# Kernel optimization log

Measured on AMD Instinct MI355X. Metric: run time of the kernel, lower is better.

## Reference

```python
import jax, jax.numpy as jnp
import numpy as np
from jax import lax

B, C_IN, C_OUT, T = 2048, 64, 64, 32
E = 32768
K_HOPS = 2
KSIZE = 3
EPS = 1e-5
SLOPE = 0.01  # torch LeakyReLU default negative_slope


def setup_inputs() -> dict:
    key = jax.random.key(0)
    ks = jax.random.split(key, 10)
    x = jax.random.normal(ks[0], (B, C_IN, T), dtype=jnp.float32)
    edge_index = jax.random.randint(ks[1], (2, E), 0, B, dtype=jnp.int64)
    edge_weight = jax.random.uniform(ks[2], (E,), dtype=jnp.float32)
    # temporal Conv1d params: weight [out, in, k], bias [out]
    conv_w = jax.random.normal(ks[3], (C_OUT, C_IN, KSIZE), dtype=jnp.float32) / np.sqrt(C_IN * KSIZE)
    conv_b = jnp.zeros((C_OUT,), dtype=jnp.float32)
    # LayerNorm([out_channels, T]) elementwise affine over last two dims
    ln_g = jnp.ones((C_OUT, T), dtype=jnp.float32)
    ln_b = jnp.zeros((C_OUT, T), dtype=jnp.float32)
    # BatchNorm1d over node features inside residual layer (res+ pre-norm)
    bn_g = jnp.ones((C_OUT,), dtype=jnp.float32)
    bn_b = jnp.zeros((C_OUT,), dtype=jnp.float32)
    # TAGConv: one linear per hop (K+1 of them) plus bias
    tag_w = jax.random.normal(ks[4], (K_HOPS + 1, C_OUT, C_OUT), dtype=jnp.float32) / np.sqrt(C_OUT)
    tag_b = jnp.zeros((C_OUT,), dtype=jnp.float32)
    return {
        'x': x, 'edge_index': edge_index, 'edge_weight': edge_weight,
        'conv_w': conv_w, 'conv_b': conv_b, 'ln_g': ln_g, 'ln_b': ln_b,
        'bn_g': bn_g, 'bn_b': bn_b, 'tag_w': tag_w, 'tag_b': tag_b,
    }


def _forward(x, edge_index, edge_weight, conv_w, conv_b, ln_g, ln_b, bn_g, bn_b, tag_w, tag_b):
    Bn, Cin, Tn = x.shape
    # --- Temporal1DConvLayer: Conv1d with padding=k-1 both sides, truncate to T, pool='none', LeakyReLU ---
    y = lax.conv_general_dilated(x, conv_w, window_strides=(1,),
                                 padding=[(KSIZE - 1, KSIZE - 1)],
                                 dimension_numbers=('NCH', 'OIH', 'NCH'))
    y = y + conv_b[None, :, None]
    y = y[..., :Tn]                                   # [B, C_out, T]
    y = jnp.where(y >= 0, y, SLOPE * y)               # LeakyReLU
    # --- temporal_norm_layer: LayerNorm over (C_out, T) jointly ---
    mu = jnp.mean(y, axis=(1, 2), keepdims=True)
    var = jnp.var(y, axis=(1, 2), keepdims=True)
    y = (y - mu) * lax.rsqrt(var + EPS) * ln_g[None] + ln_b[None]
    # --- parallelize over time: permute(2,0,1) -> [T, B, F]; edges replicated per t ---
    h_in = jnp.transpose(y, (2, 0, 1))                # [T, B, F]
    # --- ResidualLayer (res+): h = h_in + TAGConv(LeakyReLU(BatchNorm(h_in))) ---
    mu_n = jnp.mean(h_in, axis=(0, 1))                # batch stats over all T*B node copies
    var_n = jnp.var(h_in, axis=(0, 1))
    z = (h_in - mu_n) * lax.rsqrt(var_n + EPS) * bn_g + bn_b
    z = jnp.where(z >= 0, z, SLOPE * z)
    src, dst = edge_index[0], edge_index[1]
    out = jnp.einsum('tbf,fg->tbg', z, tag_w[0])
    p = z
    for k in range(1, K_HOPS + 1):
        msg = p[:, src, :] * edge_weight[None, :, None]   # [T, E, F] gather
        p = jnp.zeros_like(p).at[:, dst, :].add(msg)      # scatter-add per timestep
        out = out + jnp.einsum('tbf,fg->tbg', p, tag_w[k])
    out = out + tag_b
    h = h_in + out                                    # residual 'res+'
    # --- reshape back: [T, B, F] -> [B, F, T] ---
    return jnp.transpose(h, (1, 2, 0))


def reference(x, edge_index, edge_weight, conv_w, conv_b, ln_g, ln_b, bn_g, bn_b, tag_w, tag_b):
    return _forward(x, edge_index, edge_weight, conv_w, conv_b, ln_g, ln_b, bn_g, bn_b, tag_w, tag_b)
```

## Files before the change

### kernel.cpp

```cpp
#include <hip/hip_runtime.h>
#include <cstddef>

#define NB   2048
#define NE   32768
#define NTC  2048
#define SLOPE_F 0.01f
#define EPS_F   1e-5f

typedef short bf16x8 __attribute__((ext_vector_type(8)));
typedef float f32x4  __attribute__((ext_vector_type(4)));

__device__ __forceinline__ unsigned short f2bf(float f) {
    unsigned u = __builtin_bit_cast(unsigned, f);
    u += 0x7FFF + ((u >> 16) & 1);
    return (unsigned short)(u >> 16);
}
__device__ __forceinline__ float bflo(unsigned v) {
    return __builtin_bit_cast(float, v << 16);
}
__device__ __forceinline__ float bfhi(unsigned v) {
    return __builtin_bit_cast(float, v & 0xFFFF0000u);
}
__device__ __forceinline__ unsigned pk2(float lo, float hi) {
    return (unsigned)f2bf(lo) | ((unsigned)f2bf(hi) << 16);
}
__device__ __forceinline__ void accv8(float* acc, const uint4& v, float wt) {
    acc[0] += wt * bflo(v.x); acc[1] += wt * bfhi(v.x);
    acc[2] += wt * bflo(v.y); acc[3] += wt * bfhi(v.y);
    acc[4] += wt * bflo(v.z); acc[5] += wt * bfhi(v.z);
    acc[6] += wt * bflo(v.w); acc[7] += wt * bfhi(v.w);
}
__device__ __forceinline__ void acci16(float* acc, const uint4& v, float wt) {
    acc[0] += wt * (float)(short)(v.x & 0xFFFFu); acc[1] += wt * (float)(short)(v.x >> 16);
    acc[2] += wt * (float)(short)(v.y & 0xFFFFu); acc[3] += wt * (float)(short)(v.y >> 16);
    acc[4] += wt * (float)(short)(v.z & 0xFFFFu); acc[5] += wt * (float)(short)(v.z >> 16);
    acc[6] += wt * (float)(short)(v.w & 0xFFFFu); acc[7] += wt * (float)(short)(v.w >> 16);
}
__device__ __forceinline__ unsigned pkq2(float a, float b, float inv) {
    int qa = __float2int_rn(a * inv);
    int qb = __float2int_rn(b * inv);
    return ((unsigned)qa & 0xFFFFu) | ((unsigned)qb << 16);
}
__device__ __forceinline__ void spl2(float a, float b, unsigned& hw, unsigned& lw) {
    unsigned short ha = f2bf(a), hb = f2bf(b);
    float ra = a - bflo((unsigned)ha);
    float rb = b - bflo((unsigned)hb);
    hw = (unsigned)ha | ((unsigned)hb << 16);
    lw = (unsigned)f2bf(ra) | ((unsigned)f2bf(rb) << 16);
}

__device__ __forceinline__ int edge_src(const int* ei, int m, int e) {
    return m ? ei[e] : ei[2 * e];
}
__device__ __forceinline__ int edge_dst(const int* ei, int m, int e) {
    return m ? ei[NE + e] : ei[2 * (NE + e)];
}

__global__ __launch_bounds__(256)
void k_pre(int* __restrict__ hist, const float* __restrict__ cw,
           unsigned short* __restrict__ wAb, const float* __restrict__ tw,
           unsigned short* __restrict__ twB, unsigned short* __restrict__ twBlo)
{
    int gid = blockIdx.x * 256 + threadIdx.x;
    if (gid < 2048) hist[gid] = 0;
    if (blockIdx.x < 48) {
        int idx = gid;
        int kk = idx >> 12, o = (idx >> 6) & 63, i = idx & 63;
        wAb[idx] = f2bf(cw[o * 192 + i * 3 + kk]);
    } else if (blockIdx.x < 96) {
        int idx = gid - 48 * 256;
        int mm = idx >> 12, rem = idx & 4095;
        int g = rem >> 6, k = rem & 63;
        twB[idx] = f2bf(tw[mm * 4096 + k * 64 + g]);
    } else {
        int idx = gid - 96 * 256;
        int g = idx >> 6, k = idx & 63;
        float v = tw[2 * 4096 + k * 64 + g];
        unsigned short hi = f2bf(v);
        twBlo[idx] = f2bf(v - bflo((unsigned)hi));
    }
}

__global__ __launch_bounds__(256, 4)
void k_main(const float* __restrict__ x, const unsigned short* __restrict__ wAb,
            const float* __restrict__ cb, const float* __restrict__ lg,
            const float* __restrict__ lb, float* __restrict__ h_in,
            float* __restrict__ partials,
            const int* __restrict__ ei, int* __restrict__ hist)
{
    if (blockIdx.x >= NB) {
        int e = (blockIdx.x - NB) * 256 + threadIdx.x;
        unsigned long long bal = __ballot(ei[2 * e + 1] != 0);
        int m = (bal != 0ull) ? 1 : 0;
        atomicAdd(&hist[edge_dst(ei, m, e)], 1);
        return;
    }
    __shared__ __align__(16) unsigned short xT[36 * 72];
    __shared__ float hT[32 * 65];
    __shared__ float red1[64], red2[64];
    __shared__ float wsum[8];
    __shared__ float bcast[2];

    const int b = blockIdx.x, j = threadIdx.x;
    const float* __restrict__ xg = x + (size_t)b * NTC;

    {
        unsigned* xTd = (unsigned*)xT;
        int t = j & 31, p = j >> 5;
#pragma unroll
        for (int r = 0; r < 4; ++r) {
            int i0 = (r * 8 + p) * 2;
            float v0 = xg[i0 * 32 + t];
            float v1 = xg[(i0 + 1) * 32 + t];
            xTd[(t + 2) * 36 + (i0 >> 1)] = pk2(v0, v1);
        }
        if (j < 72)       xTd[j] = 0u;
        else if (j < 144) xTd[1224 + (j - 72)] = 0u;
    }
    __syncthreads();

    const int lane = j & 63, w = j >> 6;
    const int n16 = lane & 15, quad = lane >> 4;

    bf16x8 afr[3][2];
#pragma unroll
    for (int kk = 0; kk < 3; ++kk)
#pragma unroll
        for (int s = 0; s < 2; ++s) {
            int off16 = (kk * 64 + w * 16 + n16) * 64 + s * 32 + quad * 8;
            afr[kk][s] = *(const bf16x8*)(wAb + off16);
        }

    f32x4 acc0 = {0.f, 0.f, 0.f, 0.f};
    f32x4 acc1 = {0.f, 0.f, 0.f, 0.f};
#pragma unroll
    for (int kk = 0; kk < 3; ++kk)
#pragma unroll
        for (int s = 0; s < 2; ++s) {
            bf16x8 b0 = *(const bf16x8*)(xT + (n16 + kk) * 72 + s * 32 + quad * 8);
            bf16x8 b1 = *(const bf16x8*)(xT + (16 + n16 + kk) * 72 + s * 32 + quad * 8);
            acc0 = __builtin_amdgcn_mfma_f32_16x16x32_bf16(afr[kk][s], b0, acc0, 0, 0, 0);
            acc1 = __builtin_amdgcn_mfma_f32_16x16x32_bf16(afr[kk][s], b1, acc1, 0, 0, 0);
        }

    float vals[2][4];
    float s1 = 0.f, s2 = 0.f;
#pragma unroll
    for (int r = 0; r < 4; ++r) {
        float cbv = cb[w * 16 + quad * 4 + r];
        float v0 = acc0[r] + cbv;
        float v1 = acc1[r] + cbv;
        v0 = (v0 >= 0.f) ? v0 : SLOPE_F * v0;
        v1 = (v1 >= 0.f) ? v1 : SLOPE_F * v1;
        vals[0][r] = v0; vals[1][r] = v1;
        s1 += v0 + v1; s2 += v0 * v0 + v1 * v1;
    }
#pragma unroll
    for (int off = 32; off > 0; off >>= 1) {
        s1 += __shfl_down(s1, off, 64);
        s2 += __shfl_down(s2, off, 64);
    }
    if (lane == 0) { wsum[w] = s1; wsum[4 + w] = s2; }
    __syncthreads();
    if (j == 0) {
        float S1 = wsum[0] + wsum[1] + wsum[2] + wsum[3];
        float S2 = wsum[4] + wsum[5] + wsum[6] + wsum[7];
        float mu  = S1 * (1.f / 2048.f);
        float var = S2 * (1.f / 2048.f) - mu * mu;
        bcast[0] = mu;
        bcast[1] = rsqrtf(var + EPS_F);
    }
    __syncthreads();
    const float mu = bcast[0], rs = bcast[1];
    float po1[4] = {0.f, 0.f, 0.f, 0.f}, po2[4] = {0.f, 0.f, 0.f, 0.f};
#pragma unroll
    for (int nt = 0; nt < 2; ++nt) {
        int t = nt * 16 + n16;
#pragma unroll
        for (int r = 0; r < 4; ++r) {
            int o = w * 16 + quad * 4 + r;
            float h = (vals[nt][r] - mu) * rs * lg[o * 32 + t] + lb[o * 32 + t];
            hT[t * 65 + o] = h;
            po1[r] += h; po2[r] += h * h;
        }
    }
#pragma unroll
    for (int off = 8; off > 0; off >>= 1) {
#pragma unroll
        for (int r = 0; r < 4; ++r) {
            po1[r] += __shfl_down(po1[r], off, 16);
            po2[r] += __shfl_down(po2[r], off, 16);
        }
    }
    if (n16 == 0) {
#pragma unroll
        for (int r = 0; r < 4; ++r) {
            int o = w * 16 + quad * 4 + r;
            red1[o] = po1[r];
            red2[o] = po2[r];
        }
    }
    __syncthreads();
    float* hb = h_in + (size_t)b * NTC;
#pragma unroll
    for (int r = 0; r < 8; ++r) {
        int idx = j + r * 256;
        hb[idx] = hT[(idx >> 6) * 65 + (idx & 63)];
    }
    float* pb_ = partials + (size_t)b * 128;
    if (j < 64)       pb_[j] = red1[j];
    else if (j < 128) pb_[j] = red2[j - 64];
}

__global__ __launch_bounds__(256)
void k_mid(const int* __restrict__ hist, int* __restrict__ rowp,
           int* __restrict__ cur, const float* __restrict__ partials,
           const float* __restrict__ bg, const float* __restrict__ bb,
           float* __restrict__ stats)
{
    __shared__ int part[256];
    __shared__ float r1[4], r2[4];
    const int j = threadIdx.x;
    if (blockIdx.x == 0) {
        int loc[8]; int s = 0;
#pragma unroll
        for (int r = 0; r < 8; ++r) { loc[r] = hist[j * 8 + r]; s += loc[r]; }
        part[j] = s;
        __syncthreads();
        for (int off = 1; off < 256; off <<= 1) {
            int v = (j >= off) ? part[j - off] : 0;
            __syncthreads();
            part[j] += v;
            __syncthreads();
        }
        int excl = part[j] - s;
#pragma unroll
        for (int r = 0; r < 8; ++r) {
            rowp[j * 8 + r] = excl;
            cur [j * 8 + r] = excl;
            excl += loc[r];
        }
        if (j == 255) rowp[2048] = excl;
        return;
    }
    const int c = blockIdx.x - 1;
    float s1 = 0.f, s2 = 0.f;
    for (int b = j; b < NB; b += 256) {
        const float* p = partials + (size_t)b * 128;
        s1 += p[c];
        s2 += p[64 + c];
    }
#pragma unroll
    for (int off = 32; off > 0; off >>= 1) {
        s1 += __shfl_down(s1, off, 64);
        s2 += __shfl_down(s2, off, 64);
    }
    if ((j & 63) == 0) { r1[j >> 6] = s1; r2[j >> 6] = s2; }
    __syncthreads();
    if (j == 0) {
        float S1 = r1[0] + r1[1] + r1[2] + r1[3];
        float S2 = r2[0] + r2[1] + r2[2] + r2[3];
        const float inv_n = 1.f / 65536.f;
        float mu  = S1 * inv_n;
        float var = S2 * inv_n - mu * mu;
        float rs  = rsqrtf(var + EPS_F);
        float sc  = bg[c] * rs;
        stats[128 + c] = sc;
        stats[192 + c] = bb[c] - mu * sc;
    }
}

__global__ __launch_bounds__(256)
void k_zs(const float* __restrict__ h_in, const float* __restrict__ stats,
          unsigned short* __restrict__ zb16,
          const int* __restrict__ ei, const float* __restrict__ ew,
          int* __restrict__ cur, int* __restrict__ csrs, float* __restrict__ csrw)
{
    const int j = threadIdx.x;
    if (blockIdx.x >= NB) {
        int e = (blockIdx.x - NB) * 256 + j;
        unsigned long long bal = __ballot(ei[2 * e + 1] != 0);
        int m = (bal != 0ull) ? 1 : 0;
        int d = edge_dst(ei, m, e);
        int pos = atomicAdd(&cur[d], 1);
        csrs[pos] = edge_src(ei, m, e);
        csrw[pos] = ew[e];
        return;
    }
    __shared__ float scs[64], shs[64];
    const int b = blockIdx.x;
    if (j < 64)        scs[j] = stats[128 + j];
    else if (j < 128)  shs[j - 64] = stats[192 + (j - 64)];
    __syncthreads();
    const float4* hb = (const float4*)(h_in + (size_t)b * NTC);
    float4 a = hb[2 * j], c4 = hb[2 * j + 1];
    const int c0 = (j * 8) & 63;
    float z0 = a.x  * scs[c0+0] + shs[c0+0];
    float z1 = a.y  * scs[c0+1] + shs[c0+1];
    float z2 = a.z  * scs[c0+2] + shs[c0+2];
    float z3 = a.w  * scs[c0+3] + shs[c0+3];
    float z4 = c4.x * scs[c0+4] + shs[c0+4];
    float z5 = c4.y * scs[c0+5] + shs[c0+5];
    float z6 = c4.z * scs[c0+6] + shs[c0+6];
    float z7 = c4.w * scs[c0+7] + shs[c0+7];
    z0 = (z0 >= 0.f) ? z0 : SLOPE_F * z0;  z1 = (z1 >= 0.f) ? z1 : SLOPE_F * z1;
    z2 = (z2 >= 0.f) ? z2 : SLOPE_F * z2;  z3 = (z3 >= 0.f) ? z3 : SLOPE_F * z3;
    z4 = (z4 >= 0.f) ? z4 : SLOPE_F * z4;  z5 = (z5 >= 0.f) ? z5 : SLOPE_F * z5;
    z6 = (z6 >= 0.f) ? z6 : SLOPE_F * z6;  z7 = (z7 >= 0.f) ? z7 : SLOPE_F * z7;
    uint4 q;
    q.x = pk2(z0, z1); q.y = pk2(z2, z3); q.z = pk2(z4, z5); q.w = pk2(z6, z7);
    ((uint4*)(zb16 + (size_t)b * NTC))[j] = q;
}

__global__ __launch_bounds__(256, 4)
void k_hop1(const unsigned short* __restrict__ p_in, const float* __restrict__ h_in,
            const int* __restrict__ rowp, const int* __restrict__ csrs,
            const float* __restrict__ csrw, const unsigned short* __restrict__ twB,
            const float* __restrict__ tb,
            unsigned short* __restrict__ p1q, float* __restrict__ p1scl,
            float* __restrict__ out)
{
    __shared__ __align__(16) unsigned short pA[32 * 64];
    __shared__ __align__(16) unsigned short zA[32 * 64];
    __shared__ float hl[32 * 65];
    __shared__ float mred[4];
    const int d = blockIdx.x, j = threadIdx.x;

    {
        uint4 zv = ((const uint4*)(p_in + (size_t)d * NTC))[j];
        ((uint4*)zA)[j] = zv;
        const float4* hb4 = (const float4*)(h_in + (size_t)d * NTC);
        float4 h0 = hb4[2 * j], h1 = hb4[2 * j + 1];
        int tt = j >> 3, c0 = (j & 7) * 8;
        float* q = &hl[tt * 65 + c0];
        q[0] = h0.x; q[1] = h0.y; q[2] = h0.z; q[3] = h0.w;
        q[4] = h1.x; q[5] = h1.y; q[6] = h1.z; q[7] = h1.w;
    }

    const int beg = rowp[d], end = rowp[d + 1];
    float acc[8];
#pragma unroll
    for (int r = 0; r < 8; ++r) acc[r] = 0.f;
    int e = beg;
    for (; e + 8 <= end; e += 8) {
        int   s0 = csrs[e],   s1 = csrs[e+1], s2 = csrs[e+2], s3 = csrs[e+3];
        int   s4 = csrs[e+4], s5 = csrs[e+5], s6 = csrs[e+6], s7 = csrs[e+7];
        float w0 = csrw[e],   w1 = csrw[e+1], w2 = csrw[e+2], w3 = csrw[e+3];
        float w4 = csrw[e+4], w5 = csrw[e+5], w6 = csrw[e+6], w7 = csrw[e+7];
        uint4 v0 = ((const uint4*)(p_in + (size_t)s0 * NTC))[j];
        uint4 v1 = ((const uint4*)(p_in + (size_t)s1 * NTC))[j];
        uint4 v2 = ((const uint4*)(p_in + (size_t)s2 * NTC))[j];
        uint4 v3 = ((const uint4*)(p_in + (size_t)s3 * NTC))[j];
        uint4 v4 = ((const uint4*)(p_in + (size_t)s4 * NTC))[j];
        uint4 v5 = ((const uint4*)(p_in + (size_t)s5 * NTC))[j];
        uint4 v6 = ((const uint4*)(p_in + (size_t)s6 * NTC))[j];
        uint4 v7 = ((const uint4*)(p_in + (size_t)s7 * NTC))[j];
        accv8(acc, v0, w0); accv8(acc, v1, w1);
        accv8(acc, v2, w2); accv8(acc, v3, w3);
        accv8(acc, v4, w4); accv8(acc, v5, w5);
        accv8(acc, v6, w6); accv8(acc, v7, w7);
    }
    for (; e + 2 <= end; e += 2) {
        int s0 = csrs[e],  s1 = csrs[e+1];
        float w0 = csrw[e], w1 = csrw[e+1];
        uint4 v0 = ((const uint4*)(p_in + (size_t)s0 * NTC))[j];
        uint4 v1 = ((const uint4*)(p_in + (size_t)s1 * NTC))[j];
        accv8(acc, v0, w0); accv8(acc, v1, w1);
    }
    if (e < end) {
        int s0 = csrs[e];
        float w0 = csrw[e];
        uint4 v0 = ((const uint4*)(p_in + (size_t)s0 * NTC))[j];
        accv8(acc, v0, w0);
    }

    const int lane = j & 63, w = j >> 6;
    float m = 0.f;
#pragma unroll
    for (int r = 0; r < 8; ++r) m = fmaxf(m, fabsf(acc[r]));
#pragma unroll
    for (int off = 32; off > 0; off >>= 1)
        m = fmaxf(m, __shfl_down(m, off, 64));
    if (lane == 0) mred[w] = m;
    __syncthreads();
    const float mv = fmaxf(fmaxf(mred[0], mred[1]), fmaxf(mred[2], mred[3]));
    const float inv = (mv > 0.f) ? (32767.f / mv) : 0.f;
    if (j == 0) p1scl[d] = mv * (1.f / 32767.f);

    {
        uint4 qv;
        qv.x = pkq2(acc[0], acc[1], inv);
        qv.y = pkq2(acc[2], acc[3], inv);
        qv.z = pkq2(acc[4], acc[5], inv);
        qv.w = pkq2(acc[6], acc[7], inv);
        ((uint4*)(p1q + (size_t)d * NTC))[j] = qv;
    }
    uint4 pv;
    pv.x = pk2(acc[0], acc[1]); pv.y = pk2(acc[2], acc[3]);
    pv.z = pk2(acc[4], acc[5]); pv.w = pk2(acc[6], acc[7]);
    ((uint4*)pA)[j] = pv;
    __syncthreads();

    const int n16 = lane & 15, quad = lane >> 4;
    const int g = w * 16 + n16;

    bf16x8 za00 = *(const bf16x8*)(zA + (n16)      * 64 +      quad * 8);
    bf16x8 za01 = *(const bf16x8*)(zA + (n16)      * 64 + 32 + quad * 8);
    bf16x8 za10 = *(const bf16x8*)(zA + (16 + n16) * 64 +      quad * 8);
    bf16x8 za11 = *(const bf16x8*)(zA + (16 + n16) * 64 + 32 + quad * 8);
    bf16x8 pa00 = *(const bf16x8*)(pA + (n16)      * 64 +      quad * 8);
    bf16x8 pa01 = *(const bf16x8*)(pA + (n16)      * 64 + 32 + quad * 8);
    bf16x8 pa10 = *(const bf16x8*)(pA + (16 + n16) * 64 +      quad * 8);
    bf16x8 pa11 = *(const bf16x8*)(pA + (16 + n16) * 64 + 32 + quad * 8);
    bf16x8 b0w0 = *(const bf16x8*)(twB + g * 64 +      quad * 8);
    bf16x8 b1w0 = *(const bf16x8*)(twB + g * 64 + 32 + quad * 8);
    bf16x8 b0w1 = *(const bf16x8*)(twB + 4096 + g * 64 +      quad * 8);
    bf16x8 b1w1 = *(const bf16x8*)(twB + 4096 + g * 64 + 32 + quad * 8);

    f32x4 d0 = {0.f, 0.f, 0.f, 0.f};
    f32x4 d1 = {0.f, 0.f, 0.f, 0.f};
    d0 = __builtin_amdgcn_mfma_f32_16x16x32_bf16(za00, b0w0, d0, 0, 0, 0);
    d0 = __builtin_amdgcn_mfma_f32_16x16x32_bf16(za01, b1w0, d0, 0, 0, 0);
    d0 = __builtin_amdgcn_mfma_f32_16x16x32_bf16(pa00, b0w1, d0, 0, 0, 0);
    d0 = __builtin_amdgcn_mfma_f32_16x16x32_bf16(pa01, b1w1, d0, 0, 0, 0);
    d1 = __builtin_amdgcn_mfma_f32_16x16x32_bf16(za10, b0w0, d1, 0, 0, 0);
    d1 = __builtin_amdgcn_mfma_f32_16x16x32_bf16(za11, b1w0, d1, 0, 0, 0);
    d1 = __builtin_amdgcn_mfma_f32_16x16x32_bf16(pa10, b0w1, d1, 0, 0, 0);
    d1 = __builtin_amdgcn_mfma_f32_16x16x32_bf16(pa11, b1w1, d1, 0, 0, 0);

    const float tbg = tb[g];
    float* ob = out + (size_t)d * NTC + g * 32;
    {
        float4 v;
        v.x = d0[0] + tbg + hl[(quad * 4 + 0) * 65 + g];
        v.y = d0[1] + tbg + hl[(quad * 4 + 1) * 65 + g];
        v.z = d0[2] + tbg + hl[(quad * 4 + 2) * 65 + g];
        v.w = d0[3] + tbg + hl[(quad * 4 + 3) * 65 + g];
        *(float4*)(ob + quad * 4) = v;
    }
    {
        float4 v;
        v.x = d1[0] + tbg + hl[(16 + quad * 4 + 0) * 65 + g];
        v.y = d1[1] + tbg + hl[(16 + quad * 4 + 1) * 65 + g];
        v.z = d1[2] + tbg + hl[(16 + quad * 4 + 2) * 65 + g];
        v.w = d1[3] + tbg + hl[(16 + quad * 4 + 3) * 65 + g];
        *(float4*)(ob + 16 + quad * 4) = v;
    }
}

__global__ __launch_bounds__(256, 4)
void k_hop2(const unsigned short* __restrict__ p1q, const float* __restrict__ p1scl,
            const int* __restrict__ rowp, const int* __restrict__ csrs,
            const float* __restrict__ csrw,
            const unsigned short* __restrict__ twB2,
            const unsigned short* __restrict__ twB2lo,
            float* __restrict__ out)
{
    __shared__ __align__(16) unsigned short pH[32 * 64];
    __shared__ __align__(16) unsigned short pL[32 * 64];
    const int d = blockIdx.x, j = threadIdx.x;
    const int beg = rowp[d], end = rowp[d + 1];
    float acc[8];
#pragma unroll
    for (int r = 0; r < 8; ++r) acc[r] = 0.f;
    int e = beg;
    for (; e + 8 <= end; e += 8) {
        int   s0 = csrs[e],   s1 = csrs[e+1], s2 = csrs[e+2], s3 = csrs[e+3];
        int   s4 = csrs[e+4], s5 = csrs[e+5], s6 = csrs[e+6], s7 = csrs[e+7];
        float w0 = csrw[e]   * p1scl[s0];
        float w1 = csrw[e+1] * p1scl[s1];
        float w2 = csrw[e+2] * p1scl[s2];
        float w3 = csrw[e+3] * p1scl[s3];
        float w4 = csrw[e+4] * p1scl[s4];
        float w5 = csrw[e+5] * p1scl[s5];
        float w6 = csrw[e+6] * p1scl[s6];
        float w7 = csrw[e+7] * p1scl[s7];
        uint4 v0 = ((const uint4*)(p1q + (size_t)s0 * NTC))[j];
        uint4 v1 = ((const uint4*)(p1q + (size_t)s1 * NTC))[j];
        uint4 v2 = ((const uint4*)(p1q + (size_t)s2 * NTC))[j];
        uint4 v3 = ((const uint4*)(p1q + (size_t)s3 * NTC))[j];
        uint4 v4 = ((const uint4*)(p1q + (size_t)s4 * NTC))[j];
        uint4 v5 = ((const uint4*)(p1q + (size_t)s5 * NTC))[j];
        uint4 v6 = ((const uint4*)(p1q + (size_t)s6 * NTC))[j];
        uint4 v7 = ((const uint4*)(p1q + (size_t)s7 * NTC))[j];
        acci16(acc, v0, w0); acci16(acc, v1, w1);
        acci16(acc, v2, w2); acci16(acc, v3, w3);
        acci16(acc, v4, w4); acci16(acc, v5, w5);
        acci16(acc, v6, w6); acci16(acc, v7, w7);
    }
    for (; e + 2 <= end; e += 2) {
        int s0 = csrs[e],  s1 = csrs[e+1];
        float w0 = csrw[e]   * p1scl[s0];
        float w1 = csrw[e+1] * p1scl[s1];
        uint4 v0 = ((const uint4*)(p1q + (size_t)s0 * NTC))[j];
        uint4 v1 = ((const uint4*)(p1q + (size_t)s1 * NTC))[j];
        acci16(acc, v0, w0); acci16(acc, v1, w1);
    }
    if (e < end) {
        int s0 = csrs[e];
        float w0 = csrw[e] * p1scl[s0];
        uint4 v0 = ((const uint4*)(p1q + (size_t)s0 * NTC))[j];
        acci16(acc, v0, w0);
    }
    {
        uint4 qh, ql;
        spl2(acc[0], acc[1], qh.x, ql.x);
        spl2(acc[2], acc[3], qh.y, ql.y);
        spl2(acc[4], acc[5], qh.z, ql.z);
        spl2(acc[6], acc[7], qh.w, ql.w);
        ((uint4*)pH)[j] = qh;
        ((uint4*)pL)[j] = ql;
    }
    __syncthreads();

    const int lane = j & 63, w = j >> 6;
    const int n16 = lane & 15, quad = lane >> 4;
    const int g = w * 16 + n16;

    bf16x8 ah00 = *(const bf16x8*)(pH + (n16)      * 64 +      quad * 8);
    bf16x8 ah01 = *(const bf16x8*)(pH + (n16)      * 64 + 32 + quad * 8);
    bf16x8 ah10 = *(const bf16x8*)(pH + (16 + n16) * 64 +      quad * 8);
    bf16x8 ah11 = *(const bf16x8*)(pH + (16 + n16) * 64 + 32 + quad * 8);
    bf16x8 al00 = *(const bf16x8*)(pL + (n16)      * 64 +      quad * 8);
    bf16x8 al01 = *(const bf16x8*)(pL + (n16)      * 64 + 32 + quad * 8);
    bf16x8 al10 = *(const bf16x8*)(pL + (16 + n16) * 64 +      quad * 8);
    bf16x8 al11 = *(const bf16x8*)(pL + (16 + n16) * 64 + 32 + quad * 8);
    bf16x8 b0h  = *(const bf16x8*)(twB2   + g * 64 +      quad * 8);
    bf16x8 b1h  = *(const bf16x8*)(twB2   + g * 64 + 32 + quad * 8);
    bf16x8 b0l  = *(const bf16x8*)(twB2lo + g * 64 +      quad * 8);
    bf16x8 b1l  = *(const bf16x8*)(twB2lo + g * 64 + 32 + quad * 8);

    f32x4 d0 = {0.f, 0.f, 0.f, 0.f};
    f32x4 d1 = {0.f, 0.f, 0.f, 0.f};
    d0 = __builtin_amdgcn_mfma_f32_16x16x32_bf16(ah00, b0h, d0, 0, 0, 0);
    d0 = __builtin_amdgcn_mfma_f32_16x16x32_bf16(ah01, b1h, d0, 0, 0, 0);
    d1 = __builtin_amdgcn_mfma_f32_16x16x32_bf16(ah10, b0h, d1, 0, 0, 0);
    d1 = __builtin_amdgcn_mfma_f32_16x16x32_bf16(ah11, b1h, d1, 0, 0, 0);
    d0 = __builtin_amdgcn_mfma_f32_16x16x32_bf16(ah00, b0l, d0, 0, 0, 0);
    d0 = __builtin_amdgcn_mfma_f32_16x16x32_bf16(ah01, b1l, d0, 0, 0, 0);
    d1 = __builtin_amdgcn_mfma_f32_16x16x32_bf16(ah10, b0l, d1, 0, 0, 0);
    d1 = __builtin_amdgcn_mfma_f32_16x16x32_bf16(ah11, b1l, d1, 0, 0, 0);
    d0 = __builtin_amdgcn_mfma_f32_16x16x32_bf16(al00, b0h, d0, 0, 0, 0);
    d0 = __builtin_amdgcn_mfma_f32_16x16x32_bf16(al01, b1h, d0, 0, 0, 0);
    d1 = __builtin_amdgcn_mfma_f32_16x16x32_bf16(al10, b0h, d1, 0, 0, 0);
    d1 = __builtin_amdgcn_mfma_f32_16x16x32_bf16(al11, b1h, d1, 0, 0, 0);

    float* ob = out + (size_t)d * NTC + g * 32;
    {
        float4 v = *(float4*)(ob + quad * 4);
        v.x += d0[0]; v.y += d0[1]; v.z += d0[2]; v.w += d0[3];
        *(float4*)(ob + quad * 4) = v;
    }
    {
        float4 v = *(float4*)(ob + 16 + quad * 4);
        v.x += d1[0]; v.y += d1[1]; v.z += d1[2]; v.w += d1[3];
        *(float4*)(ob + 16 + quad * 4) = v;
    }
}

extern "C" void kernel_launch(void* const* d_in, const int* in_sizes, int n_in,
                              void* d_out, int out_size, void* d_ws, size_t ws_size,
                              hipStream_t stream)
{
    const float* x  = (const float*)d_in[0];
    const int*   ei = (const int*)  d_in[1];
    const float* ew = (const float*)d_in[2];
    const float* cw = (const float*)d_in[3];
    const float* cb = (const float*)d_in[4];
    const float* lg = (const float*)d_in[5];
    const float* lb = (const float*)d_in[6];
    const float* bg = (const float*)d_in[7];
    const float* bb = (const float*)d_in[8];
    const float* tw = (const float*)d_in[9];
    const float* tb = (const float*)d_in[10];
    float* out = (float*)d_out;
    float* ws  = (float*)d_ws;

    float*          h_in  = ws;
    unsigned short* p1q   = (unsigned short*)(ws + 4194304);
    float*          p1scl = ws + 6291456;
    unsigned short* zbf   = (unsigned short*)(ws + 8388608);
    float*          stats = ws + 10485760;
    unsigned short* wAb   = (unsigned short*)(ws + 10486016);
    unsigned short* twB   = (unsigned short*)(ws + 10492160);
    float*          parts = ws + 10498304;
    int*            ib    = (int*)(ws + 10760448);
    unsigned short* twBlo = (unsigned short*)(ws + 10832640);
    int*   hist  = ib;
    int*   rowp  = ib + 2048;
    int*   cur   = ib + 4100;
    int*   csrs  = ib + 6148;
    float* csrw  = (float*)(ib + 38916);

    k_pre  <<<112,      256, 0, stream>>>(hist, cw, wAb, tw, twB, twBlo);
    k_main <<<NB + 128, 256, 0, stream>>>(x, wAb, cb, lg, lb, h_in, parts, ei, hist);
    k_mid  <<<65,       256, 0, stream>>>(hist, rowp, cur, parts, bg, bb, stats);
    k_zs   <<<NB + 128, 256, 0, stream>>>(h_in, stats, zbf, ei, ew, cur, csrs, csrw);
    k_hop1 <<<NB,       256, 0, stream>>>(zbf, h_in, rowp, csrs, csrw, twB, tb, p1q, p1scl, out);
    k_hop2 <<<NB,       256, 0, stream>>>(p1q, p1scl, rowp, csrs, csrw, twB + 8192, twBlo, out);
}
```

Baseline: 163.0 us.

## Move hop-0/hop-1 matmuls and residual into hop2 to write output once

k_hop1 now only gathers neighbours and writes the quantized hop-1 features, dropping its shared buffers, MFMA work and output write, and raising its occupancy hint. k_hop2 reloads z, h_in and the dequantized hop-1 features and performs all three hop matmuls plus bias and residual in one pass, writing the output once. This removes one full read-modify-write of the output buffer and lightens the gather-bound hop1 kernel. In exchange hop2 uses more shared memory and registers, and hop-1 now reaches the matmul through the int16 quantization rather than directly as bf16.

```diff
diff --git a/kernel.cpp b/kernel.cpp
--- a/kernel.cpp
+++ b/kernel.cpp
@@ -312,31 +312,13 @@
     ((uint4*)(zb16 + (size_t)b * NTC))[j] = q;
 }
 
-__global__ __launch_bounds__(256, 4)
-void k_hop1(const unsigned short* __restrict__ p_in, const float* __restrict__ h_in,
-            const int* __restrict__ rowp, const int* __restrict__ csrs,
-            const float* __restrict__ csrw, const unsigned short* __restrict__ twB,
-            const float* __restrict__ tb,
-            unsigned short* __restrict__ p1q, float* __restrict__ p1scl,
-            float* __restrict__ out)
-{
-    __shared__ __align__(16) unsigned short pA[32 * 64];
-    __shared__ __align__(16) unsigned short zA[32 * 64];
-    __shared__ float hl[32 * 65];
+__global__ __launch_bounds__(256, 6)
+void k_hop1(const unsigned short* __restrict__ p_in, const int* __restrict__ rowp,
+            const int* __restrict__ csrs, const float* __restrict__ csrw,
+            unsigned short* __restrict__ p1q, float* __restrict__ p1scl)
+{
     __shared__ float mred[4];
     const int d = blockIdx.x, j = threadIdx.x;
-
-    {
-        uint4 zv = ((const uint4*)(p_in + (size_t)d * NTC))[j];
-        ((uint4*)zA)[j] = zv;
-        const float4* hb4 = (const float4*)(h_in + (size_t)d * NTC);
-        float4 h0 = hb4[2 * j], h1 = hb4[2 * j + 1];
-        int tt = j >> 3, c0 = (j & 7) * 8;
-        float* q = &hl[tt * 65 + c0];
-        q[0] = h0.x; q[1] = h0.y; q[2] = h0.z; q[3] = h0.w;
-        q[4] = h1.x; q[5] = h1.y; q[6] = h1.z; q[7] = h1.w;
-    }
-
     const int beg = rowp[d], end = rowp[d + 1];
     float acc[8];
 #pragma unroll
@@ -387,78 +369,50 @@
     const float inv = (mv > 0.f) ? (32767.f / mv) : 0.f;
     if (j == 0) p1scl[d] = mv * (1.f / 32767.f);
 
-    {
-        uint4 qv;
-        qv.x = pkq2(acc[0], acc[1], inv);
-        qv.y = pkq2(acc[2], acc[3], inv);
-        qv.z = pkq2(acc[4], acc[5], inv);
-        qv.w = pkq2(acc[6], acc[7], inv);
-        ((uint4*)(p1q + (size_t)d * NTC))[j] = qv;
-    }
-    uint4 pv;
-    pv.x = pk2(acc[0], acc[1]); pv.y = pk2(acc[2], acc[3]);
-    pv.z = pk2(acc[4], acc[5]); pv.w = pk2(acc[6], acc[7]);
-    ((uint4*)pA)[j] = pv;
-    __syncthreads();
-
-    const int n16 = lane & 15, quad = lane >> 4;
-    const int g = w * 16 + n16;
-
-    bf16x8 za00 = *(const bf16x8*)(zA + (n16)      * 64 +      quad * 8);
-    bf16x8 za01 = *(const bf16x8*)(zA + (n16)      * 64 + 32 + quad * 8);
-    bf16x8 za10 = *(const bf16x8*)(zA + (16 + n16) * 64 +      quad * 8);
-    bf16x8 za11 = *(const bf16x8*)(zA + (16 + n16) * 64 + 32 + quad * 8);
-    bf16x8 pa00 = *(const bf16x8*)(pA + (n16)      * 64 +      quad * 8);
-    bf16x8 pa01 = *(const bf16x8*)(pA + (n16)      * 64 + 32 + quad * 8);
-    bf16x8 pa10 = *(const bf16x8*)(pA + (16 + n16) * 64 +      quad * 8);
-    bf16x8 pa11 = *(const bf16x8*)(pA + (16 + n16) * 64 + 32 + quad * 8);
-    bf16x8 b0w0 = *(const bf16x8*)(twB + g * 64 +      quad * 8);
-    bf16x8 b1w0 = *(const bf16x8*)(twB + g * 64 + 32 + quad * 8);
-    bf16x8 b0w1 = *(const bf16x8*)(twB + 4096 + g * 64 +      quad * 8);
-    bf16x8 b1w1 = *(const bf16x8*)(twB + 4096 + g * 64 + 32 + quad * 8);
-
-    f32x4 d0 = {0.f, 0.f, 0.f, 0.f};
-    f32x4 d1 = {0.f, 0.f, 0.f, 0.f};
-    d0 = __builtin_amdgcn_mfma_f32_16x16x32_bf16(za00, b0w0, d0, 0, 0, 0);
-    d0 = __builtin_amdgcn_mfma_f32_16x16x32_bf16(za01, b1w0, d0, 0, 0, 0);
-    d0 = __builtin_amdgcn_mfma_f32_16x16x32_bf16(pa00, b0w1, d0, 0, 0, 0);
-    d0 = __builtin_amdgcn_mfma_f32_16x16x32_bf16(pa01, b1w1, d0, 0, 0, 0);
-    d1 = __builtin_amdgcn_mfma_f32_16x16x32_bf16(za10, b0w0, d1, 0, 0, 0);
-    d1 = __builtin_amdgcn_mfma_f32_16x16x32_bf16(za11, b1w0, d1, 0, 0, 0);
-    d1 = __builtin_amdgcn_mfma_f32_16x16x32_bf16(pa10, b0w1, d1, 0, 0, 0);
-    d1 = __builtin_amdgcn_mfma_f32_16x16x32_bf16(pa11, b1w1, d1, 0, 0, 0);
-
-    const float tbg = tb[g];
-    float* ob = out + (size_t)d * NTC + g * 32;
-    {
-        float4 v;
-        v.x = d0[0] + tbg + hl[(quad * 4 + 0) * 65 + g];
-        v.y = d0[1] + tbg + hl[(quad * 4 + 1) * 65 + g];
-        v.z = d0[2] + tbg + hl[(quad * 4 + 2) * 65 + g];
-        v.w = d0[3] + tbg + hl[(quad * 4 + 3) * 65 + g];
-        *(float4*)(ob + quad * 4) = v;
-    }
-    {
-        float4 v;
-        v.x = d1[0] + tbg + hl[(16 + quad * 4 + 0) * 65 + g];
-        v.y = d1[1] + tbg + hl[(16 + quad * 4 + 1) * 65 + g];
-        v.z = d1[2] + tbg + hl[(16 + quad * 4 + 2) * 65 + g];
-        v.w = d1[3] + tbg + hl[(16 + quad * 4 + 3) * 65 + g];
-        *(float4*)(ob + 16 + quad * 4) = v;
-    }
+    uint4 qv;
+    qv.x = pkq2(acc[0], acc[1], inv);
+    qv.y = pkq2(acc[2], acc[3], inv);
+    qv.z = pkq2(acc[4], acc[5], inv);
+    qv.w = pkq2(acc[6], acc[7], inv);
+    ((uint4*)(p1q + (size_t)d * NTC))[j] = qv;
 }
 
 __global__ __launch_bounds__(256, 4)
 void k_hop2(const unsigned short* __restrict__ p1q, const float* __restrict__ p1scl,
+            const unsigned short* __restrict__ zb16, const float* __restrict__ h_in,
             const int* __restrict__ rowp, const int* __restrict__ csrs,
             const float* __restrict__ csrw,
-            const unsigned short* __restrict__ twB2,
+            const unsigned short* __restrict__ twB,
             const unsigned short* __restrict__ twB2lo,
+            const float* __restrict__ tb,
             float* __restrict__ out)
 {
+    __shared__ __align__(16) unsigned short zA[32 * 64];
+    __shared__ __align__(16) unsigned short pA[32 * 64];
     __shared__ __align__(16) unsigned short pH[32 * 64];
     __shared__ __align__(16) unsigned short pL[32 * 64];
+    __shared__ float hl[32 * 65];
     const int d = blockIdx.x, j = threadIdx.x;
+
+    {
+        uint4 zv = ((const uint4*)(zb16 + (size_t)d * NTC))[j];
+        ((uint4*)zA)[j] = zv;
+        const float4* hb4 = (const float4*)(h_in + (size_t)d * NTC);
+        float4 h0 = hb4[2 * j], h1 = hb4[2 * j + 1];
+        int tt = j >> 3, c0 = (j & 7) * 8;
+        float* q = &hl[tt * 65 + c0];
+        q[0] = h0.x; q[1] = h0.y; q[2] = h0.z; q[3] = h0.w;
+        q[4] = h1.x; q[5] = h1.y; q[6] = h1.z; q[7] = h1.w;
+        uint4 pq = ((const uint4*)(p1q + (size_t)d * NTC))[j];
+        const float scl = p1scl[d];
+        uint4 pb;
+        pb.x = pk2(scl * (float)(short)(pq.x & 0xFFFFu), scl * (float)(short)(pq.x >> 16));
+        pb.y = pk2(scl * (float)(short)(pq.y & 0xFFFFu), scl * (float)(short)(pq.y >> 16));
+        pb.z = pk2(scl * (float)(short)(pq.z & 0xFFFFu), scl * (float)(short)(pq.z >> 16));
+        pb.w = pk2(scl * (float)(short)(pq.w & 0xFFFFu), scl * (float)(short)(pq.w >> 16));
+        ((uint4*)pA)[j] = pb;
+    }
+
     const int beg = rowp[d], end = rowp[d + 1];
     float acc[8];
 #pragma unroll
@@ -517,43 +471,75 @@
     const int n16 = lane & 15, quad = lane >> 4;
     const int g = w * 16 + n16;
 
-    bf16x8 ah00 = *(const bf16x8*)(pH + (n16)      * 64 +      quad * 8);
-    bf16x8 ah01 = *(const bf16x8*)(pH + (n16)      * 64 + 32 + quad * 8);
-    bf16x8 ah10 = *(const bf16x8*)(pH + (16 + n16) * 64 +      quad * 8);
-    bf16x8 ah11 = *(const bf16x8*)(pH + (16 + n16) * 64 + 32 + quad * 8);
-    bf16x8 al00 = *(const bf16x8*)(pL + (n16)      * 64 +      quad * 8);
-    bf16x8 al01 = *(const bf16x8*)(pL + (n16)      * 64 + 32 + quad * 8);
-    bf16x8 al10 = *(const bf16x8*)(pL + (16 + n16) * 64 +      quad * 8);
-    bf16x8 al11 = *(const bf16x8*)(pL + (16 + n16) * 64 + 32 + quad * 8);
-    bf16x8 b0h  = *(const bf16x8*)(twB2   + g * 64 +      quad * 8);
-    bf16x8 b1h  = *(const bf16x8*)(twB2   + g * 64 + 32 + quad * 8);
-    bf16x8 b0l  = *(const bf16x8*)(twB2lo + g * 64 +      quad * 8);
-    bf16x8 b1l  = *(const bf16x8*)(twB2lo + g * 64 + 32 + quad * 8);
-
     f32x4 d0 = {0.f, 0.f, 0.f, 0.f};
     f32x4 d1 = {0.f, 0.f, 0.f, 0.f};
-    d0 = __builtin_amdgcn_mfma_f32_16x16x32_bf16(ah00, b0h, d0, 0, 0, 0);
-    d0 = __builtin_amdgcn_mfma_f32_16x16x32_bf16(ah01, b1h, d0, 0, 0, 0);
-    d1 = __builtin_amdgcn_mfma_f32_16x16x32_bf16(ah10, b0h, d1, 0, 0, 0);
-    d1 = __builtin_amdgcn_mfma_f32_16x16x32_bf16(ah11, b1h, d1, 0, 0, 0);
-    d0 = __builtin_amdgcn_mfma_f32_16x16x32_bf16(ah00, b0l, d0, 0, 0, 0);
-    d0 = __builtin_amdgcn_mfma_f32_16x16x32_bf16(ah01, b1l, d0, 0, 0, 0);
-    d1 = __builtin_amdgcn_mfma_f32_16x16x32_bf16(ah10, b0l, d1, 0, 0, 0);
-    d1 = __builtin_amdgcn_mfma_f32_16x16x32_bf16(ah11, b1l, d1, 0, 0, 0);
-    d0 = __builtin_amdgcn_mfma_f32_16x16x32_bf16(al00, b0h, d0, 0, 0, 0);
-    d0 = __builtin_amdgcn_mfma_f32_16x16x32_bf16(al01, b1h, d0, 0, 0, 0);
-    d1 = __builtin_amdgcn_mfma_f32_16x16x32_bf16(al10, b0h, d1, 0, 0, 0);
-    d1 = __builtin_amdgcn_mfma_f32_16x16x32_bf16(al11, b1h, d1, 0, 0, 0);
-
+    {
+        bf16x8 a00 = *(const bf16x8*)(zA + (n16)      * 64 +      quad * 8);
+        bf16x8 a01 = *(const bf16x8*)(zA + (n16)      * 64 + 32 + quad * 8);
+        bf16x8 a10 = *(const bf16x8*)(zA + (16 + n16) * 64 +      quad * 8);
+        bf16x8 a11 = *(const bf16x8*)(zA + (16 + n16) * 64 + 32 + quad * 8);
+        bf16x8 b0  = *(const bf16x8*)(twB + g * 64 +      quad * 8);
+        bf16x8 b1  = *(const bf16x8*)(twB + g * 64 + 32 + quad * 8);
+        d0 = __builtin_amdgcn_mfma_f32_16x16x32_bf16(a00, b0, d0, 0, 0, 0);
+        d0 = __builtin_amdgcn_mfma_f32_16x16x32_bf16(a01, b1, d0, 0, 0, 0);
+        d1 = __builtin_amdgcn_mfma_f32_16x16x32_bf16(a10, b0, d1, 0, 0, 0);
+        d1 = __builtin_amdgcn_mfma_f32_16x16x32_bf16(a11, b1, d1, 0, 0, 0);
+    }
+    {
+        bf16x8 a00 = *(const bf16x8*)(pA + (n16)      * 64 +      quad * 8);
+        bf16x8 a01 = *(const bf16x8*)(pA + (n16)      * 64 + 32 + quad * 8);
+        bf16x8 a10 = *(const bf16x8*)(pA + (16 + n16) * 64 +      quad * 8);
+        bf16x8 a11 = *(const bf16x8*)(pA + (16 + n16) * 64 + 32 + quad * 8);
+        bf16x8 b0  = *(const bf16x8*)(twB + 4096 + g * 64 +      quad * 8);
+        bf16x8 b1  = *(const bf16x8*)(twB + 4096 + g * 64 + 32 + quad * 8);
+        d0 = __builtin_amdgcn_mfma_f32_16x16x32_bf16(a00, b0, d0, 0, 0, 0);
+        d0 = __builtin_amdgcn_mfma_f32_16x16x32_bf16(a01, b1, d0, 0, 0, 0);
+        d1 = __builtin_amdgcn_mfma_f32_16x16x32_bf16(a10, b0, d1, 0, 0, 0);
+        d1 = __builtin_amdgcn_mfma_f32_16x16x32_bf16(a11, b1, d1, 0, 0, 0);
+    }
+    {
+        bf16x8 ah00 = *(const bf16x8*)(pH + (n16)      * 64 +      quad * 8);
+        bf16x8 ah01 = *(const bf16x8*)(pH + (n16)      * 64 + 32 + quad * 8);
+        bf16x8 ah10 = *(const bf16x8*)(pH + (16 + n16) * 64 +      quad * 8);
+        bf16x8 ah11 = *(const bf16x8*)(pH + (16 + n16) * 64 + 32 + quad * 8);
+        bf16x8 b0h  = *(const bf16x8*)(twB + 8192 + g * 64 +      quad * 8);
+        bf16x8 b1h  = *(const bf16x8*)(twB + 8192 + g * 64 + 32 + quad * 8);
+        d0 = __builtin_amdgcn_mfma_f32_16x16x32_bf16(ah00, b0h, d0, 0, 0, 0);
+        d0 = __builtin_amdgcn_mfma_f32_16x16x32_bf16(ah01, b1h, d0, 0, 0, 0);
+        d1 = __builtin_amdgcn_mfma_f32_16x16x32_bf16(ah10, b0h, d1, 0, 0, 0);
+        d1 = __builtin_amdgcn_mfma_f32_16x16x32_bf16(ah11, b1h, d1, 0, 0, 0);
+        bf16x8 b0l  = *(const bf16x8*)(twB2lo + g * 64 +      quad * 8);
+        bf16x8 b1l  = *(const bf16x8*)(twB2lo + g * 64 + 32 + quad * 8);
+        d0 = __builtin_amdgcn_mfma_f32_16x16x32_bf16(ah00, b0l, d0, 0, 0, 0);
+        d0 = __builtin_amdgcn_mfma_f32_16x16x32_bf16(ah01, b1l, d0, 0, 0, 0);
+        d1 = __builtin_amdgcn_mfma_f32_16x16x32_bf16(ah10, b0l, d1, 0, 0, 0);
+        d1 = __builtin_amdgcn_mfma_f32_16x16x32_bf16(ah11, b1l, d1, 0, 0, 0);
+        bf16x8 al00 = *(const bf16x8*)(pL + (n16)      * 64 +      quad * 8);
+        bf16x8 al01 = *(const bf16x8*)(pL + (n16)      * 64 + 32 + quad * 8);
+        bf16x8 al10 = *(const bf16x8*)(pL + (16 + n16) * 64 +      quad * 8);
+        bf16x8 al11 = *(const bf16x8*)(pL + (16 + n16) * 64 + 32 + quad * 8);
+        d0 = __builtin_amdgcn_mfma_f32_16x16x32_bf16(al00, b0h, d0, 0, 0, 0);
+        d0 = __builtin_amdgcn_mfma_f32_16x16x32_bf16(al01, b1h, d0, 0, 0, 0);
+        d1 = __builtin_amdgcn_mfma_f32_16x16x32_bf16(al10, b0h, d1, 0, 0, 0);
+        d1 = __builtin_amdgcn_mfma_f32_16x16x32_bf16(al11, b1h, d1, 0, 0, 0);
+    }
+
+    const float tbg = tb[g];
     float* ob = out + (size_t)d * NTC + g * 32;
     {
-        float4 v = *(float4*)(ob + quad * 4);
-        v.x += d0[0]; v.y += d0[1]; v.z += d0[2]; v.w += d0[3];
+        float4 v;
+        v.x = d0[0] + tbg + hl[(quad * 4 + 0) * 65 + g];
+        v.y = d0[1] + tbg + hl[(quad * 4 + 1) * 65 + g];
+        v.z = d0[2] + tbg + hl[(quad * 4 + 2) * 65 + g];
+        v.w = d0[3] + tbg + hl[(quad * 4 + 3) * 65 + g];
         *(float4*)(ob + quad * 4) = v;
     }
     {
-        float4 v = *(float4*)(ob + 16 + quad * 4);
-        v.x += d1[0]; v.y += d1[1]; v.z += d1[2]; v.w += d1[3];
+        float4 v;
+        v.x = d1[0] + tbg + hl[(16 + quad * 4 + 0) * 65 + g];
+        v.y = d1[1] + tbg + hl[(16 + quad * 4 + 1) * 65 + g];
+        v.z = d1[2] + tbg + hl[(16 + quad * 4 + 2) * 65 + g];
+        v.w = d1[3] + tbg + hl[(16 + quad * 4 + 3) * 65 + g];
         *(float4*)(ob + 16 + quad * 4) = v;
     }
 }
@@ -596,6 +582,7 @@
     k_main <<<NB + 128, 256, 0, stream>>>(x, wAb, cb, lg, lb, h_in, parts, ei, hist);
     k_mid  <<<65,       256, 0, stream>>>(hist, rowp, cur, parts, bg, bb, stats);
     k_zs   <<<NB + 128, 256, 0, stream>>>(h_in, stats, zbf, ei, ew, cur, csrs, csrw);
-    k_hop1 <<<NB,       256, 0, stream>>>(zbf, h_in, rowp, csrs, csrw, twB, tb, p1q, p1scl, out);
-    k_hop2 <<<NB,       256, 0, stream>>>(p1q, p1scl, rowp, csrs, csrw, twB + 8192, twBlo, out);
-}
+    k_hop1 <<<NB,       256, 0, stream>>>(zbf, rowp, csrs, csrw, p1q, p1scl);
+    k_hop2 <<<NB,       256, 0, stream>>>(p1q, p1scl, zbf, h_in, rowp, csrs, csrw,
+                                          twB, twBlo, tb, out);
+}
```

After: 159.7 us. -2.1%, faster.
